# Optimization experiments

Hardware: AMD Instinct MI355X
Metric: run time of the kernel (lower is better)

## Reference

```python
import jax, jax.numpy as jnp
import numpy as np

EMBED_DIM = 512
NUM_HEADS = 8
HEAD_DIM = EMBED_DIM // NUM_HEADS
SCALE = HEAD_DIM ** -0.5
TEMP = 1.0


def setup_inputs() -> dict:
    key = jax.random.key(0)
    ks = jax.random.split(key, 12)
    B, N, Nk, C = 4, 2048, 2048, EMBED_DIM
    s = C ** -0.5
    return {
        "x": jax.random.normal(ks[0], (B, N, C), jnp.float32),
        "y": jax.random.normal(ks[1], (B, Nk, C), jnp.float32),
        "z": jax.random.normal(ks[2], (B, Nk, C), jnp.float32),
        "Wq": jax.random.normal(ks[3], (C, C), jnp.float32) * s,
        "bq": jnp.zeros((C,), jnp.float32),
        "Wk": jax.random.normal(ks[4], (C, C), jnp.float32) * s,
        "bk": jnp.zeros((C,), jnp.float32),
        "Wv": jax.random.normal(ks[5], (C, C), jnp.float32) * s,
        "bv": jnp.zeros((C,), jnp.float32),
        "Wo": jax.random.normal(ks[6], (C, C), jnp.float32) * s,
        "bo": jnp.zeros((C,), jnp.float32),
    }


def reference(x, y, z, Wq, bq, Wk, bk, Wv, bv, Wo, bo):
    B, N, C = x.shape
    Nk = y.shape[1]
    H, D = NUM_HEADS, HEAD_DIM

    def split_heads(t, L):
        return t.reshape(B, L, H, D).transpose(0, 2, 1, 3)  # [B,H,L,D]

    q = split_heads(x @ Wq.T + bq, N)
    k = split_heads(y @ Wk.T + bk, Nk)
    v = split_heads(z @ Wv.T + bv, Nk)

    # [B,H,N,Nk] logits, scaled
    logits = jnp.einsum("bhnd,bhkd->bhnk", q, k) * SCALE

    # Gumbel-softmax (soft, tau=TEMP) with a fixed noise key
    gkey = jax.random.key(42)
    gumbels = jax.random.gumbel(gkey, logits.shape, logits.dtype)
    attn = jax.nn.softmax((logits + gumbels) / TEMP, axis=-1)

    out = jnp.einsum("bhnk,bhkd->bhnd", attn, v)
    out = out.transpose(0, 2, 1, 3).reshape(B, N, C)
    return out @ Wo.T + bo
```

## Files before the change

kernel.cpp:

```cpp
#include <hip/hip_runtime.h>
#include <hip/hip_bf16.h>
#include <stdint.h>

#define Bdim 4
#define Hdim 8
#define Ndim 2048
#define Cdim 512
#define Ddim 64
#define SCALE_F 0.125f
#define KSPLIT 4
#define LOG2E 1.44269504f
#define QSCALE_F (SCALE_F * LOG2E)

typedef __bf16 bf16_t;
typedef __bf16 bf16x8 __attribute__((ext_vector_type(8)));
typedef float f32x4 __attribute__((ext_vector_type(4)));

__device__ __forceinline__ void gumbel_tile(uint32_t base, float (&pf)[4][4]) {
  const uint32_t k1 = 42u, k2 = 0x1BD11BDAu ^ 42u;
  uint32_t s0[16], s1[16];
#pragma unroll
  for (int i = 0; i < 16; i++) {
    s0[i] = 0u;
    s1[i] = base + ((uint32_t)(i >> 2) << 11) + (uint32_t)((i & 3) * 16);
  }
#define TF_RND(rot)                                                    \
  {                                                                    \
    _Pragma("unroll") for (int i = 0; i < 16; i++) {                   \
      s0[i] += s1[i];                                                  \
      s1[i] = __builtin_rotateleft32(s1[i], (rot)) ^ s0[i];            \
    }                                                                  \
  }
#define TF_INJ(a, b)                                                   \
  {                                                                    \
    _Pragma("unroll") for (int i = 0; i < 16; i++) {                   \
      s0[i] += (a);                                                    \
      s1[i] += (b);                                                    \
    }                                                                  \
  }
#define TF_INJ1(b)                                                     \
  {                                                                    \
    _Pragma("unroll") for (int i = 0; i < 16; i++) { s1[i] += (b); }   \
  }
  TF_RND(13) TF_RND(15) TF_RND(26) TF_RND(6)
  TF_INJ(k1, k2 + 1u)
  TF_RND(17) TF_RND(29) TF_RND(16) TF_RND(24)
  TF_INJ(k2, 2u)
  TF_RND(13) TF_RND(15) TF_RND(26) TF_RND(6)
  TF_INJ1(k1 + 3u)
  TF_RND(17) TF_RND(29) TF_RND(16) TF_RND(24)
  TF_INJ(k1, k2 + 4u)
  TF_RND(13) TF_RND(15) TF_RND(26) TF_RND(6)
  TF_INJ(k2, 5u)
#undef TF_RND
#undef TF_INJ
#undef TF_INJ1
#pragma unroll
  for (int i = 0; i < 16; i++) {
    uint32_t bits = s0[i] ^ s1[i];
    uint32_t mant;
    asm("v_alignbit_b32 %0, %1, %2, 9" : "=v"(mant) : "s"(127u), "v"(bits));
    float u = __uint_as_float(mant) - 1.0f;
    pf[i >> 2][i & 3] = -__builtin_amdgcn_rcpf(__builtin_amdgcn_logf(u));
  }
}

__device__ __forceinline__ void stage8_f32(bf16_t* dst, const float* src) {
  float4 a0 = *(const float4*)src;
  float4 a1 = *(const float4*)(src + 4);
  union { bf16_t h[8]; uint4 u; } pk;
  pk.h[0] = (bf16_t)a0.x; pk.h[1] = (bf16_t)a0.y;
  pk.h[2] = (bf16_t)a0.z; pk.h[3] = (bf16_t)a0.w;
  pk.h[4] = (bf16_t)a1.x; pk.h[5] = (bf16_t)a1.y;
  pk.h[6] = (bf16_t)a1.z; pk.h[7] = (bf16_t)a1.w;
  *(uint4*)dst = pk.u;
}

template <bool AF32, bool WF32>
__device__ __forceinline__ void gemm_core_t(const void* __restrict__ Av,
                                            const void* __restrict__ Wv,
                                            int m0, int n0,
                                            bf16_t* As, bf16_t* Ws,
                                            f32x4 (&acc)[4][4]) {
  const int t = threadIdx.x;
  const int wave = t >> 6, lane = t & 63;
  const int ln = lane & 15, qd = lane >> 4;
  const int wm = wave >> 1, wn = wave & 1;

#pragma unroll
  for (int i = 0; i < 4; i++)
#pragma unroll
    for (int j = 0; j < 4; j++) acc[i][j] = (f32x4){0.f, 0.f, 0.f, 0.f};

  for (int kt = 0; kt < Cdim / 64; ++kt) {
#pragma unroll
    for (int it = 0; it < 4; ++it) {
      int vec = it * 256 + t;
      int row = vec >> 3, c8 = (vec & 7) * 8;
      if constexpr (AF32)
        stage8_f32(&As[row * 72 + c8],
                   (const float*)Av + (size_t)(m0 + row) * Cdim + kt * 64 + c8);
      else
        *(bf16x8*)&As[row * 72 + c8] =
            *((const bf16x8*)Av + ((size_t)(m0 + row) * Cdim + kt * 64 + c8) / 8);
      if constexpr (WF32)
        stage8_f32(&Ws[row * 72 + c8],
                   (const float*)Wv + (size_t)(n0 + row) * Cdim + kt * 64 + c8);
      else
        *(bf16x8*)&Ws[row * 72 + c8] =
            *((const bf16x8*)Wv + ((size_t)(n0 + row) * Cdim + kt * 64 + c8) / 8);
    }
    __syncthreads();
#pragma unroll
    for (int ks = 0; ks < 2; ++ks) {
      bf16x8 af[4], bfr[4];
#pragma unroll
      for (int i = 0; i < 4; i++)
        af[i] = *(const bf16x8*)&As[(wm * 64 + i * 16 + ln) * 72 + ks * 32 + qd * 8];
#pragma unroll
      for (int j = 0; j < 4; j++)
        bfr[j] = *(const bf16x8*)&Ws[(wn * 64 + j * 16 + ln) * 72 + ks * 32 + qd * 8];
#pragma unroll
      for (int i = 0; i < 4; i++)
#pragma unroll
        for (int j = 0; j < 4; j++)
          acc[i][j] = __builtin_amdgcn_mfma_f32_16x16x32_bf16(af[i], bfr[j],
                                                              acc[i][j], 0, 0, 0);
    }
    __syncthreads();
  }
}

__global__ __launch_bounds__(256, 3)
void qkv_gemm_kernel(const float* __restrict__ x, const float* __restrict__ y,
                     const float* __restrict__ z, const float* __restrict__ Wq,
                     const float* __restrict__ Wk, const float* __restrict__ Wv,
                     const float* __restrict__ bq, const float* __restrict__ bk,
                     const float* __restrict__ bv, bf16_t* __restrict__ qo,
                     bf16_t* __restrict__ ko, bf16_t* __restrict__ vo) {
  __shared__ bf16_t As[128 * 72];
  __shared__ bf16_t Ws[128 * 72];
  const int sel = blockIdx.z;
  const float* A = sel == 0 ? x : (sel == 1 ? y : z);
  const float* W = sel == 0 ? Wq : (sel == 1 ? Wk : Wv);
  const float* bias = sel == 0 ? bq : (sel == 1 ? bk : bv);
  bf16_t* O = sel == 0 ? qo : (sel == 1 ? ko : vo);
  const float mul = sel == 0 ? QSCALE_F : 1.0f;
  const int m0 = blockIdx.y * 128, n0 = blockIdx.x * 128;

  f32x4 acc[4][4];
  gemm_core_t<true, true>(A, W, m0, n0, As, Ws, acc);

  const int t = threadIdx.x;
  const int wave = t >> 6, lane = t & 63;
  const int ln = lane & 15, qd = lane >> 4;
  const int wm = wave >> 1, wn = wave & 1;
#pragma unroll
  for (int i = 0; i < 4; i++)
#pragma unroll
    for (int j = 0; j < 4; j++)
#pragma unroll
      for (int r = 0; r < 4; r++) {
        int grow = m0 + wm * 64 + i * 16 + qd * 4 + r;
        int gcol = n0 + wn * 64 + j * 16 + ln;
        float val = (acc[i][j][r] + bias[gcol]) * mul;
        int b = grow >> 11, n = grow & 2047;
        int h = gcol >> 6, d = gcol & 63;
        O[(((size_t)b * Hdim + h) * Ndim + n) * Ddim + d] = (bf16_t)val;
      }
}

__global__ __launch_bounds__(256, 4)
void out_gemm_kernel(const bf16_t* __restrict__ ab, const float* __restrict__ Wo,
                     const float* __restrict__ bo, float* __restrict__ out) {
  __shared__ bf16_t As[128 * 72];
  __shared__ bf16_t Ws[64 * 72];
  const int t = threadIdx.x;
  const int wave = t >> 6, lane = t & 63;
  const int ln = lane & 15, qd = lane >> 4;
  const int wm = wave >> 1, wn = wave & 1;
  const int m0 = blockIdx.y * 128, n0 = blockIdx.x * 64;

  f32x4 acc[4][2];
#pragma unroll
  for (int i = 0; i < 4; i++)
#pragma unroll
    for (int j = 0; j < 2; j++) acc[i][j] = (f32x4){0.f, 0.f, 0.f, 0.f};

  for (int kt = 0; kt < Cdim / 64; ++kt) {
#pragma unroll
    for (int it = 0; it < 4; ++it) {
      int vec = it * 256 + t;
      int row = vec >> 3, c8 = (vec & 7) * 8;
      *(bf16x8*)&As[row * 72 + c8] =
          *(const bf16x8*)&ab[(size_t)(m0 + row) * Cdim + kt * 64 + c8];
    }
#pragma unroll
    for (int it = 0; it < 2; ++it) {
      int vec = it * 256 + t;
      int row = vec >> 3, c8 = (vec & 7) * 8;
      stage8_f32(&Ws[row * 72 + c8],
                 Wo + (size_t)(n0 + row) * Cdim + kt * 64 + c8);
    }
    __syncthreads();
#pragma unroll
    for (int ks = 0; ks < 2; ++ks) {
      bf16x8 af[4], bfr[2];
#pragma unroll
      for (int i = 0; i < 4; i++)
        af[i] = *(const bf16x8*)&As[(wm * 64 + i * 16 + ln) * 72 + ks * 32 + qd * 8];
#pragma unroll
      for (int j = 0; j < 2; j++)
        bfr[j] = *(const bf16x8*)&Ws[(wn * 32 + j * 16 + ln) * 72 + ks * 32 + qd * 8];
#pragma unroll
      for (int i = 0; i < 4; i++)
#pragma unroll
        for (int j = 0; j < 2; j++)
          acc[i][j] = __builtin_amdgcn_mfma_f32_16x16x32_bf16(af[i], bfr[j],
                                                              acc[i][j], 0, 0, 0);
    }
    __syncthreads();
  }

#pragma unroll
  for (int i = 0; i < 4; i++)
#pragma unroll
    for (int j = 0; j < 2; j++)
#pragma unroll
      for (int r = 0; r < 4; r++) {
        int grow = m0 + wm * 64 + i * 16 + qd * 4 + r;
        int gcol = n0 + wn * 32 + j * 16 + ln;
        out[(size_t)grow * Cdim + gcol] = acc[i][j][r] + bo[gcol];
      }
}

__global__ __launch_bounds__(256, 4)
void attn_kernel(const bf16_t* __restrict__ qb, const bf16_t* __restrict__ kb,
                 const bf16_t* __restrict__ vb, bf16_t* __restrict__ part_o,
                 float* __restrict__ part_l) {
  __shared__ bf16_t Ks[2][64 * 72];
  __shared__ bf16_t Vt[2][64 * 72];
  __shared__ bf16_t Ps[64 * 72];

  const int t = threadIdx.x;
  const int wave = t >> 6, lane = t & 63;
  const int ln = lane & 15, qd = lane >> 4;
  const int qtile = blockIdx.x;
  const int bh = blockIdx.y;
  const int z = blockIdx.z;
  const int qbase = qtile * 64;
  const int kt_lo = z * (Ndim / 64 / KSPLIT);
  const int kt_hi = kt_lo + (Ndim / 64 / KSPLIT);

  const bf16_t* Qg = qb + (size_t)bh * Ndim * Ddim;
  const bf16_t* Kg = kb + (size_t)bh * Ndim * Ddim;
  const bf16_t* Vg = vb + (size_t)bh * Ndim * Ddim;

  const bf16_t* Qrow = Qg + (size_t)(qbase + wave * 16 + ln) * Ddim;
  bf16x8 qf0 = *(const bf16x8*)&Qrow[qd * 8];
  bf16x8 qf1 = *(const bf16x8*)&Qrow[32 + qd * 8];

  const bf16_t one_h = (bf16_t)1.0f;
  bf16x8 ones;
#pragma unroll
  for (int i = 0; i < 8; i++) ones[i] = one_h;

  const int row0 = t >> 3,        c80 = (t & 7) * 8;
  const int row1 = (256 + t) >> 3, c81 = ((256 + t) & 7) * 8;
  const int swz0 = ((row0 >> 3) ^ (c80 >> 3)) * 8 + (row0 & 7);
  const int swz1 = ((row1 >> 3) ^ (c81 >> 3)) * 8 + (row1 & 7);

  bf16x8 kr0 = *(const bf16x8*)&Kg[(size_t)(kt_lo * 64 + row0) * Ddim + c80];
  bf16x8 kr1 = *(const bf16x8*)&Kg[(size_t)(kt_lo * 64 + row1) * Ddim + c81];
  bf16x8 vr0 = *(const bf16x8*)&Vg[(size_t)(kt_lo * 64 + row0) * Ddim + c80];
  bf16x8 vr1 = *(const bf16x8*)&Vg[(size_t)(kt_lo * 64 + row1) * Ddim + c81];

  f32x4 l_acc = (f32x4){0.f, 0.f, 0.f, 0.f};
  f32x4 o_acc[4];
#pragma unroll
  for (int j = 0; j < 4; j++) o_acc[j] = (f32x4){0.f, 0.f, 0.f, 0.f};

  const uint32_t base_rc = ((uint32_t)bh << 22) +
                           ((uint32_t)(qbase + wave * 16 + qd * 4) << 11) +
                           (uint32_t)ln + 42u;

  float pf[4][4];
  gumbel_tile(base_rc + (uint32_t)(kt_lo * 64), pf);
  *(bf16x8*)&Ks[0][row0 * 72 + c80] = kr0;
  *(bf16x8*)&Ks[0][row1 * 72 + c81] = kr1;
#pragma unroll
  for (int jj = 0; jj < 8; jj++) Vt[0][(c80 + jj) * 72 + swz0] = vr0[jj];
#pragma unroll
  for (int jj = 0; jj < 8; jj++) Vt[0][(c81 + jj) * 72 + swz1] = vr1[jj];
  __syncthreads();

  for (int kt = kt_lo; kt < kt_hi; ++kt) {
    const int cur = (kt - kt_lo) & 1;
    const bool more = kt + 1 < kt_hi;
    const bf16_t* Kc = Ks[cur];
    const bf16_t* Vc = Vt[cur];

    if (more) {
      kr0 = *(const bf16x8*)&Kg[(size_t)((kt + 1) * 64 + row0) * Ddim + c80];
      kr1 = *(const bf16x8*)&Kg[(size_t)((kt + 1) * 64 + row1) * Ddim + c81];
      vr0 = *(const bf16x8*)&Vg[(size_t)((kt + 1) * 64 + row0) * Ddim + c80];
      vr1 = *(const bf16x8*)&Vg[(size_t)((kt + 1) * 64 + row1) * Ddim + c81];
    }

    f32x4 s[4];
#pragma unroll
    for (int j = 0; j < 4; j++) s[j] = (f32x4){0.f, 0.f, 0.f, 0.f};
#pragma unroll
    for (int j = 0; j < 4; j++) {
      bf16x8 bk0 = *(const bf16x8*)&Kc[(j * 16 + ln) * 72 + qd * 8];
      bf16x8 bk1 = *(const bf16x8*)&Kc[(j * 16 + ln) * 72 + 32 + qd * 8];
      s[j] = __builtin_amdgcn_mfma_f32_16x16x32_bf16(qf0, bk0, s[j], 0, 0, 0);
      s[j] = __builtin_amdgcn_mfma_f32_16x16x32_bf16(qf1, bk1, s[j], 0, 0, 0);
    }

#pragma unroll
    for (int r = 0; r < 4; r++)
#pragma unroll
      for (int j = 0; j < 4; j++) {
        float pv = __builtin_amdgcn_exp2f(s[j][r]) * pf[r][j];
        Ps[(wave * 16 + qd * 4 + r) * 72 + j * 16 + ln] = (bf16_t)pv;
      }

#pragma unroll
    for (int ks = 0; ks < 2; ++ks) {
      bf16x8 af = *(const bf16x8*)&Ps[(wave * 16 + ln) * 72 + ks * 32 + qd * 8];
      l_acc = __builtin_amdgcn_mfma_f32_16x16x32_bf16(af, ones, l_acc, 0, 0, 0);
#pragma unroll
      for (int j = 0; j < 4; j++) {
        int d = j * 16 + ln;
        bf16x8 bv8 = *(const bf16x8*)&Vc[d * 72 + (((ks * 4 + qd) ^ (d >> 3)) << 3)];
        o_acc[j] = __builtin_amdgcn_mfma_f32_16x16x32_bf16(af, bv8, o_acc[j], 0, 0, 0);
      }
    }

    if (more) {
      gumbel_tile(base_rc + (uint32_t)((kt + 1) * 64), pf);

      bf16_t* Kn = Ks[cur ^ 1];
      bf16_t* Vn = Vt[cur ^ 1];
      *(bf16x8*)&Kn[row0 * 72 + c80] = kr0;
      *(bf16x8*)&Kn[row1 * 72 + c81] = kr1;
#pragma unroll
      for (int jj = 0; jj < 8; jj++) Vn[(c80 + jj) * 72 + swz0] = vr0[jj];
#pragma unroll
      for (int jj = 0; jj < 8; jj++) Vn[(c81 + jj) * 72 + swz1] = vr1[jj];
      __syncthreads();
    }
  }

  const int pidx = ((bh << 5) | qtile) * KSPLIT + z;
  bf16_t* po = part_o + (size_t)pidx * 64 * 64;
  float* pl = part_l + (size_t)pidx * 64;

  if (ln == 0) {
#pragma unroll
    for (int r = 0; r < 4; r++) pl[wave * 16 + qd * 4 + r] = l_acc[r];
  }
#pragma unroll
  for (int j = 0; j < 4; j++)
#pragma unroll
    for (int r = 0; r < 4; r++) {
      int row = wave * 16 + qd * 4 + r;
      int col = j * 16 + ln;
      po[row * 64 + col] = (bf16_t)o_acc[j][r];
    }
}

__global__ __launch_bounds__(256, 8)
void attn_combine(const bf16_t* __restrict__ part_o,
                  const float* __restrict__ part_l, bf16_t* __restrict__ ab) {
  const int blk = blockIdx.x;
  const int bh = blk >> 5, qtile = blk & 31;
  const int t = threadIdx.x;
  const int row = t >> 2, c0 = (t & 3) * 16;

  float l = 0.f;
#pragma unroll
  for (int zz = 0; zz < KSPLIT; zz++)
    l += part_l[(size_t)(blk * KSPLIT + zz) * 64 + row];
  const float linv = 1.0f / l;

  float acc[16];
#pragma unroll
  for (int i = 0; i < 16; i++) acc[i] = 0.f;
#pragma unroll
  for (int zz = 0; zz < KSPLIT; zz++) {
    const bf16_t* po =
        part_o + (size_t)(blk * KSPLIT + zz) * 64 * 64 + row * 64 + c0;
    bf16x8 a0 = *(const bf16x8*)&po[0];
    bf16x8 a1 = *(const bf16x8*)&po[8];
#pragma unroll
    for (int i = 0; i < 8; i++) { acc[i] += (float)a0[i]; acc[8 + i] += (float)a1[i]; }
  }

  const int b = bh >> 3, h = bh & 7;
  bf16_t* dst = ab + ((size_t)b * Ndim + qtile * 64 + row) * Cdim + h * 64 + c0;
  union { bf16_t h8[8]; uint4 u; } pk0, pk1;
#pragma unroll
  for (int i = 0; i < 8; i++) {
    pk0.h8[i] = (bf16_t)(acc[i] * linv);
    pk1.h8[i] = (bf16_t)(acc[8 + i] * linv);
  }
  *(uint4*)&dst[0] = pk0.u;
  *(uint4*)&dst[8] = pk1.u;
}

extern "C" void kernel_launch(void* const* d_in, const int* in_sizes, int n_in,
                              void* d_out, int out_size, void* d_ws, size_t ws_size,
                              hipStream_t stream) {
  const float* x  = (const float*)d_in[0];
  const float* y  = (const float*)d_in[1];
  const float* z  = (const float*)d_in[2];
  const float* Wq = (const float*)d_in[3];
  const float* bq = (const float*)d_in[4];
  const float* Wk = (const float*)d_in[5];
  const float* bk = (const float*)d_in[6];
  const float* Wv = (const float*)d_in[7];
  const float* bv = (const float*)d_in[8];
  const float* Wo = (const float*)d_in[9];
  const float* bo = (const float*)d_in[10];
  float* out = (float*)d_out;

  bf16_t* base = (bf16_t*)d_ws;
  const size_t NBIG = (size_t)Bdim * Ndim * Cdim;
  bf16_t* qb  = base;
  bf16_t* kb  = qb + NBIG;
  bf16_t* vb  = kb + NBIG;
  bf16_t* ab  = vb + NBIG;
  bf16_t* part_o = ab + NBIG;
  float* part_l = (float*)(part_o + (size_t)1024 * KSPLIT * 64 * 64);

  qkv_gemm_kernel<<<dim3(Cdim / 128, (Bdim * Ndim) / 128, 3), 256, 0, stream>>>(
      x, y, z, Wq, Wk, Wv, bq, bk, bv, qb, kb, vb);

  attn_kernel<<<dim3(Ndim / 64, Bdim * Hdim, KSPLIT), 256, 0, stream>>>(
      qb, kb, vb, part_o, part_l);

  attn_combine<<<dim3(1024), 256, 0, stream>>>(part_o, part_l, ab);

  out_gemm_kernel<<<dim3(Cdim / 64, (Bdim * Ndim) / 128), 256, 0, stream>>>(
      ab, Wo, bo, out);
}
```

Baseline: 435.6 us.

## Fuse split-K combine into output GEMM and single-buffer attention K/V tiles

```diff
diff --git a/kernel.cpp b/kernel.cpp
--- a/kernel.cpp
+++ b/kernel.cpp
@@ -171,7 +171,9 @@
 }
 
 __global__ __launch_bounds__(256, 4)
-void out_gemm_kernel(const bf16_t* __restrict__ ab, const float* __restrict__ Wo,
+void out_gemm_kernel(const bf16_t* __restrict__ part_o,
+                     const float* __restrict__ part_l,
+                     const float* __restrict__ Wo,
                      const float* __restrict__ bo, float* __restrict__ out) {
   __shared__ bf16_t As[128 * 72];
   __shared__ bf16_t Ws[64 * 72];
@@ -192,8 +194,27 @@
     for (int it = 0; it < 4; ++it) {
       int vec = it * 256 + t;
       int row = vec >> 3, c8 = (vec & 7) * 8;
-      *(bf16x8*)&As[row * 72 + c8] =
-          *(const bf16x8*)&ab[(size_t)(m0 + row) * Cdim + kt * 64 + c8];
+      int grow = m0 + row;
+      int b = grow >> 11, n = grow & 2047;
+      int qtile = n >> 6, r64 = n & 63;
+      int blk = (((b * Hdim + kt) << 5) | qtile) * KSPLIT;
+      const bf16_t* po = part_o + (size_t)blk * 4096 + r64 * 64 + c8;
+      float l = part_l[(size_t)blk * 64 + r64] +
+                part_l[(size_t)(blk + 1) * 64 + r64] +
+                part_l[(size_t)(blk + 2) * 64 + r64] +
+                part_l[(size_t)(blk + 3) * 64 + r64];
+      float linv = 1.0f / l;
+      float a8[8] = {0.f, 0.f, 0.f, 0.f, 0.f, 0.f, 0.f, 0.f};
+#pragma unroll
+      for (int zz = 0; zz < KSPLIT; zz++) {
+        bf16x8 v = *(const bf16x8*)(po + (size_t)zz * 4096);
+#pragma unroll
+        for (int i = 0; i < 8; i++) a8[i] += (float)v[i];
+      }
+      union { bf16_t h[8]; uint4 u; } pk;
+#pragma unroll
+      for (int i = 0; i < 8; i++) pk.h[i] = (bf16_t)(a8[i] * linv);
+      *(uint4*)&As[row * 72 + c8] = pk.u;
     }
 #pragma unroll
     for (int it = 0; it < 2; ++it) {
@@ -234,12 +255,12 @@
       }
 }
 
-__global__ __launch_bounds__(256, 4)
+__global__ __launch_bounds__(256, 6)
 void attn_kernel(const bf16_t* __restrict__ qb, const bf16_t* __restrict__ kb,
                  const bf16_t* __restrict__ vb, bf16_t* __restrict__ part_o,
                  float* __restrict__ part_l) {
-  __shared__ bf16_t Ks[2][64 * 72];
-  __shared__ bf16_t Vt[2][64 * 72];
+  __shared__ bf16_t Ks[64 * 72];
+  __shared__ bf16_t Vt[64 * 72];
   __shared__ bf16_t Ps[64 * 72];
 
   const int t = threadIdx.x;
@@ -286,21 +307,17 @@
 
   float pf[4][4];
   gumbel_tile(base_rc + (uint32_t)(kt_lo * 64), pf);
-  *(bf16x8*)&Ks[0][row0 * 72 + c80] = kr0;
-  *(bf16x8*)&Ks[0][row1 * 72 + c81] = kr1;
-#pragma unroll
-  for (int jj = 0; jj < 8; jj++) Vt[0][(c80 + jj) * 72 + swz0] = vr0[jj];
-#pragma unroll
-  for (int jj = 0; jj < 8; jj++) Vt[0][(c81 + jj) * 72 + swz1] = vr1[jj];
-  __syncthreads();
 
   for (int kt = kt_lo; kt < kt_hi; ++kt) {
-    const int cur = (kt - kt_lo) & 1;
-    const bool more = kt + 1 < kt_hi;
-    const bf16_t* Kc = Ks[cur];
-    const bf16_t* Vc = Vt[cur];
-
-    if (more) {
+    *(bf16x8*)&Ks[row0 * 72 + c80] = kr0;
+    *(bf16x8*)&Ks[row1 * 72 + c81] = kr1;
+#pragma unroll
+    for (int jj = 0; jj < 8; jj++) Vt[(c80 + jj) * 72 + swz0] = vr0[jj];
+#pragma unroll
+    for (int jj = 0; jj < 8; jj++) Vt[(c81 + jj) * 72 + swz1] = vr1[jj];
+    __syncthreads();
+
+    if (kt + 1 < kt_hi) {
       kr0 = *(const bf16x8*)&Kg[(size_t)((kt + 1) * 64 + row0) * Ddim + c80];
       kr1 = *(const bf16x8*)&Kg[(size_t)((kt + 1) * 64 + row1) * Ddim + c81];
       vr0 = *(const bf16x8*)&Vg[(size_t)((kt + 1) * 64 + row0) * Ddim + c80];
@@ -312,8 +329,8 @@
     for (int j = 0; j < 4; j++) s[j] = (f32x4){0.f, 0.f, 0.f, 0.f};
 #pragma unroll
     for (int j = 0; j < 4; j++) {
-      bf16x8 bk0 = *(const bf16x8*)&Kc[(j * 16 + ln) * 72 + qd * 8];
-      bf16x8 bk1 = *(const bf16x8*)&Kc[(j * 16 + ln) * 72 + 32 + qd * 8];
+      bf16x8 bk0 = *(const bf16x8*)&Ks[(j * 16 + ln) * 72 + qd * 8];
+      bf16x8 bk1 = *(const bf16x8*)&Ks[(j * 16 + ln) * 72 + 32 + qd * 8];
       s[j] = __builtin_amdgcn_mfma_f32_16x16x32_bf16(qf0, bk0, s[j], 0, 0, 0);
       s[j] = __builtin_amdgcn_mfma_f32_16x16x32_bf16(qf1, bk1, s[j], 0, 0, 0);
     }
@@ -333,24 +350,15 @@
 #pragma unroll
       for (int j = 0; j < 4; j++) {
         int d = j * 16 + ln;
-        bf16x8 bv8 = *(const bf16x8*)&Vc[d * 72 + (((ks * 4 + qd) ^ (d >> 3)) << 3)];
+        bf16x8 bv8 = *(const bf16x8*)&Vt[d * 72 + (((ks * 4 + qd) ^ (d >> 3)) << 3)];
         o_acc[j] = __builtin_amdgcn_mfma_f32_16x16x32_bf16(af, bv8, o_acc[j], 0, 0, 0);
       }
     }
 
-    if (more) {
+    if (kt + 1 < kt_hi)
       gumbel_tile(base_rc + (uint32_t)((kt + 1) * 64), pf);
 
-      bf16_t* Kn = Ks[cur ^ 1];
-      bf16_t* Vn = Vt[cur ^ 1];
-      *(bf16x8*)&Kn[row0 * 72 + c80] = kr0;
-      *(bf16x8*)&Kn[row1 * 72 + c81] = kr1;
-#pragma unroll
-      for (int jj = 0; jj < 8; jj++) Vn[(c80 + jj) * 72 + swz0] = vr0[jj];
-#pragma unroll
-      for (int jj = 0; jj < 8; jj++) Vn[(c81 + jj) * 72 + swz1] = vr1[jj];
-      __syncthreads();
-    }
+    __syncthreads();
   }
 
   const int pidx = ((bh << 5) | qtile) * KSPLIT + z;
@@ -369,45 +377,6 @@
       int col = j * 16 + ln;
       po[row * 64 + col] = (bf16_t)o_acc[j][r];
     }
-}
-
-__global__ __launch_bounds__(256, 8)
-void attn_combine(const bf16_t* __restrict__ part_o,
-                  const float* __restrict__ part_l, bf16_t* __restrict__ ab) {
-  const int blk = blockIdx.x;
-  const int bh = blk >> 5, qtile = blk & 31;
-  const int t = threadIdx.x;
-  const int row = t >> 2, c0 = (t & 3) * 16;
-
-  float l = 0.f;
-#pragma unroll
-  for (int zz = 0; zz < KSPLIT; zz++)
-    l += part_l[(size_t)(blk * KSPLIT + zz) * 64 + row];
-  const float linv = 1.0f / l;
-
-  float acc[16];
-#pragma unroll
-  for (int i = 0; i < 16; i++) acc[i] = 0.f;
-#pragma unroll
-  for (int zz = 0; zz < KSPLIT; zz++) {
-    const bf16_t* po =
-        part_o + (size_t)(blk * KSPLIT + zz) * 64 * 64 + row * 64 + c0;
-    bf16x8 a0 = *(const bf16x8*)&po[0];
-    bf16x8 a1 = *(const bf16x8*)&po[8];
-#pragma unroll
-    for (int i = 0; i < 8; i++) { acc[i] += (float)a0[i]; acc[8 + i] += (float)a1[i]; }
-  }
-
-  const int b = bh >> 3, h = bh & 7;
-  bf16_t* dst = ab + ((size_t)b * Ndim + qtile * 64 + row) * Cdim + h * 64 + c0;
-  union { bf16_t h8[8]; uint4 u; } pk0, pk1;
-#pragma unroll
-  for (int i = 0; i < 8; i++) {
-    pk0.h8[i] = (bf16_t)(acc[i] * linv);
-    pk1.h8[i] = (bf16_t)(acc[8 + i] * linv);
-  }
-  *(uint4*)&dst[0] = pk0.u;
-  *(uint4*)&dst[8] = pk1.u;
 }
 
 extern "C" void kernel_launch(void* const* d_in, const int* in_sizes, int n_in,
@@ -431,8 +400,7 @@
   bf16_t* qb  = base;
   bf16_t* kb  = qb + NBIG;
   bf16_t* vb  = kb + NBIG;
-  bf16_t* ab  = vb + NBIG;
-  bf16_t* part_o = ab + NBIG;
+  bf16_t* part_o = vb + NBIG;
   float* part_l = (float*)(part_o + (size_t)1024 * KSPLIT * 64 * 64);
 
   qkv_gemm_kernel<<<dim3(Cdim / 128, (Bdim * Ndim) / 128, 3), 256, 0, stream>>>(
@@ -441,8 +409,6 @@
   attn_kernel<<<dim3(Ndim / 64, Bdim * Hdim, KSPLIT), 256, 0, stream>>>(
       qb, kb, vb, part_o, part_l);
 
-  attn_combine<<<dim3(1024), 256, 0, stream>>>(part_o, part_l, ab);
-
   out_gemm_kernel<<<dim3(Cdim / 64, (Bdim * Ndim) / 128), 256, 0, stream>>>(
-      ab, Wo, bo, out);
-}
+      part_o, part_l, Wo, bo, out);
+}
```

After: 466.7 us. 7.1% more time.

## Replace double-buffered K/V shared tiles with single buffer and two barriers

Applied to the files above, without the earlier changes.

```diff
diff --git a/kernel.cpp b/kernel.cpp
--- a/kernel.cpp
+++ b/kernel.cpp
@@ -238,8 +238,8 @@
 void attn_kernel(const bf16_t* __restrict__ qb, const bf16_t* __restrict__ kb,
                  const bf16_t* __restrict__ vb, bf16_t* __restrict__ part_o,
                  float* __restrict__ part_l) {
-  __shared__ bf16_t Ks[2][64 * 72];
-  __shared__ bf16_t Vt[2][64 * 72];
+  __shared__ bf16_t Ks[64 * 72];
+  __shared__ bf16_t Vt[64 * 72];
   __shared__ bf16_t Ps[64 * 72];
 
   const int t = threadIdx.x;
@@ -286,21 +286,17 @@
 
   float pf[4][4];
   gumbel_tile(base_rc + (uint32_t)(kt_lo * 64), pf);
-  *(bf16x8*)&Ks[0][row0 * 72 + c80] = kr0;
-  *(bf16x8*)&Ks[0][row1 * 72 + c81] = kr1;
-#pragma unroll
-  for (int jj = 0; jj < 8; jj++) Vt[0][(c80 + jj) * 72 + swz0] = vr0[jj];
-#pragma unroll
-  for (int jj = 0; jj < 8; jj++) Vt[0][(c81 + jj) * 72 + swz1] = vr1[jj];
-  __syncthreads();
 
   for (int kt = kt_lo; kt < kt_hi; ++kt) {
-    const int cur = (kt - kt_lo) & 1;
-    const bool more = kt + 1 < kt_hi;
-    const bf16_t* Kc = Ks[cur];
-    const bf16_t* Vc = Vt[cur];
-
-    if (more) {
+    *(bf16x8*)&Ks[row0 * 72 + c80] = kr0;
+    *(bf16x8*)&Ks[row1 * 72 + c81] = kr1;
+#pragma unroll
+    for (int jj = 0; jj < 8; jj++) Vt[(c80 + jj) * 72 + swz0] = vr0[jj];
+#pragma unroll
+    for (int jj = 0; jj < 8; jj++) Vt[(c81 + jj) * 72 + swz1] = vr1[jj];
+    __syncthreads();
+
+    if (kt + 1 < kt_hi) {
       kr0 = *(const bf16x8*)&Kg[(size_t)((kt + 1) * 64 + row0) * Ddim + c80];
       kr1 = *(const bf16x8*)&Kg[(size_t)((kt + 1) * 64 + row1) * Ddim + c81];
       vr0 = *(const bf16x8*)&Vg[(size_t)((kt + 1) * 64 + row0) * Ddim + c80];
@@ -312,8 +308,8 @@
     for (int j = 0; j < 4; j++) s[j] = (f32x4){0.f, 0.f, 0.f, 0.f};
 #pragma unroll
     for (int j = 0; j < 4; j++) {
-      bf16x8 bk0 = *(const bf16x8*)&Kc[(j * 16 + ln) * 72 + qd * 8];
-      bf16x8 bk1 = *(const bf16x8*)&Kc[(j * 16 + ln) * 72 + 32 + qd * 8];
+      bf16x8 bk0 = *(const bf16x8*)&Ks[(j * 16 + ln) * 72 + qd * 8];
+      bf16x8 bk1 = *(const bf16x8*)&Ks[(j * 16 + ln) * 72 + 32 + qd * 8];
       s[j] = __builtin_amdgcn_mfma_f32_16x16x32_bf16(qf0, bk0, s[j], 0, 0, 0);
       s[j] = __builtin_amdgcn_mfma_f32_16x16x32_bf16(qf1, bk1, s[j], 0, 0, 0);
     }
@@ -333,24 +329,15 @@
 #pragma unroll
       for (int j = 0; j < 4; j++) {
         int d = j * 16 + ln;
-        bf16x8 bv8 = *(const bf16x8*)&Vc[d * 72 + (((ks * 4 + qd) ^ (d >> 3)) << 3)];
+        bf16x8 bv8 = *(const bf16x8*)&Vt[d * 72 + (((ks * 4 + qd) ^ (d >> 3)) << 3)];
         o_acc[j] = __builtin_amdgcn_mfma_f32_16x16x32_bf16(af, bv8, o_acc[j], 0, 0, 0);
       }
     }
 
-    if (more) {
+    if (kt + 1 < kt_hi)
       gumbel_tile(base_rc + (uint32_t)((kt + 1) * 64), pf);
 
-      bf16_t* Kn = Ks[cur ^ 1];
-      bf16_t* Vn = Vt[cur ^ 1];
-      *(bf16x8*)&Kn[row0 * 72 + c80] = kr0;
-      *(bf16x8*)&Kn[row1 * 72 + c81] = kr1;
-#pragma unroll
-      for (int jj = 0; jj < 8; jj++) Vn[(c80 + jj) * 72 + swz0] = vr0[jj];
-#pragma unroll
-      for (int jj = 0; jj < 8; jj++) Vn[(c81 + jj) * 72 + swz1] = vr1[jj];
-      __syncthreads();
-    }
+    __syncthreads();
   }
 
   const int pidx = ((bh << 5) | qtile) * KSPLIT + z;
```

Measured after the change: 431.7 us. Within noise of the previous version (-0.9%).
